# Kernel tuning notes

Hardware: AMD Instinct MI355X
Metric: run time of the kernel (lower is better)

## Reference

```python
import jax, jax.numpy as jnp
import numpy as np

STEPS = 250
BETA = 0.02


def setup_inputs() -> dict:
    key = jax.random.key(0)
    k1, k2 = jax.random.split(key)
    reflectance_normal = jax.random.normal(k1, (8, 1024, 1024), dtype=jnp.float32)
    distribution = jax.random.normal(k2, (8, 65536), dtype=jnp.float32)
    return {"reflectance_normal": reflectance_normal, "distribution": distribution}


def reference(reflectance_normal, distribution):
    # Faithful vectorized version of ForwardDiffusionModel.forward:
    # per batch element, 250 steps of xt = sqrt(1-b)*xt + sqrt(b)*sample,
    # where sample is drawn i.i.d. uniformly (with replacement) from the
    # flattened empirical distribution values of that batch element.
    B = reflectance_normal.shape[0]
    flat = distribution.reshape(B, -1)          # [B, N]
    N = flat.shape[1]
    a = np.sqrt(1.0 - BETA).astype(np.float32)
    b = np.sqrt(BETA).astype(np.float32)
    sample_shape = reflectance_normal.shape     # [B, H, W]

    keys = jax.random.split(jax.random.key(42), STEPS)

    def step(xt, k):
        idx = jax.random.randint(k, sample_shape, 0, N)                 # [B,H,W]
        sample = jnp.take_along_axis(flat, idx.reshape(B, -1), axis=1)  # [B,H*W]
        sample = sample.reshape(sample_shape)
        return a * xt + b * sample, None

    xt, _ = jax.lax.scan(step, reflectance_normal, keys)
    return xt
```

## Files before the change

kernel.cpp:

```cpp
#include <hip/hip_runtime.h>
#include <hip/hip_fp16.h>
#include <stdint.h>

#define NDIST 65536
#define NSTEPS 250

#define TF_ROUND(r) { x0 += x1; x1 = (x1 << (r)) | (x1 >> (32 - (r))); x1 ^= x0; }

__device__ __forceinline__ uint2 threefry2x32(uint32_t ks0, uint32_t ks1, uint32_t ks2,
                                              uint32_t x0, uint32_t x1) {
  x0 += ks0; x1 += ks1;
  TF_ROUND(13) TF_ROUND(15) TF_ROUND(26) TF_ROUND(6)
  x0 += ks1; x1 += ks2 + 1u;
  TF_ROUND(17) TF_ROUND(29) TF_ROUND(16) TF_ROUND(24)
  x0 += ks2; x1 += ks0 + 2u;
  TF_ROUND(13) TF_ROUND(15) TF_ROUND(26) TF_ROUND(6)
  x0 += ks0; x1 += ks1 + 3u;
  TF_ROUND(17) TF_ROUND(29) TF_ROUND(16) TF_ROUND(24)
  x0 += ks1; x1 += ks2 + 4u;
  TF_ROUND(13) TF_ROUND(15) TF_ROUND(26) TF_ROUND(6)
  x0 += ks2; x1 += ks0 + 5u;
  return make_uint2(x0, x1);
}

__device__ __forceinline__ void init_keys(uint32_t* keys, int tid) {
  if (tid < NSTEPS) {
    uint2 ks = threefry2x32(0u, 42u, 0x1BD11BDAu ^ 42u, 0u, (uint32_t)tid);
    uint2 k2 = threefry2x32(ks.x, ks.y, ks.x ^ ks.y ^ 0x1BD11BDAu, 0u, 1u);
    keys[2 * tid]     = k2.x;
    keys[2 * tid + 1] = k2.y;
  }
}

#define WGL 1024
#define GL  8

__global__ __launch_bounds__(WGL, 1) void fwd_diff_full(
    const float* __restrict__ x_init,
    const float* __restrict__ dist,
    float* __restrict__ out) {
  extern __shared__ char smem[];
  __half*   tab  = reinterpret_cast<__half*>(smem);
  uint32_t* keys = reinterpret_cast<uint32_t*>(smem + 131072);

  const int tid   = threadIdx.x;
  const int batch = blockIdx.x >> 7;
  const int chunk = blockIdx.x & 127;
  const uint32_t base = ((uint32_t)batch << 20) + ((uint32_t)chunk << 13);

  const float Ac = 0.9899494936611665f;
  const float Bc = 0.1414213562373095f;

  const float4* src = reinterpret_cast<const float4*>(dist + (size_t)batch * NDIST);
  for (int i = tid; i < NDIST / 4; i += WGL) {
    float4 v = src[i];
    ushort4 h;
    h.x = __half_as_ushort(__float2half(Bc * v.x));
    h.y = __half_as_ushort(__float2half(Bc * v.y));
    h.z = __half_as_ushort(__float2half(Bc * v.z));
    h.w = __half_as_ushort(__float2half(Bc * v.w));
    reinterpret_cast<ushort4*>(tab)[i] = h;
  }
  init_keys(keys, tid);
  __syncthreads();

  uint32_t p[GL];
  float acc[GL];
#pragma unroll
  for (int j = 0; j < GL; ++j) {
    p[j]   = base + (uint32_t)(j * WGL) + (uint32_t)tid;
    acc[j] = x_init[p[j]];
  }

  for (int s = 0; s < NSTEPS; ++s) {
    uint32_t kx = keys[2 * s];
    uint32_t ky = keys[2 * s + 1];
    kx = (uint32_t)__builtin_amdgcn_readfirstlane((int)kx);
    ky = (uint32_t)__builtin_amdgcn_readfirstlane((int)ky);
    const uint32_t kz = kx ^ ky ^ 0x1BD11BDAu;
#pragma unroll
    for (int j = 0; j < GL; ++j) {
      uint2 r = threefry2x32(kx, ky, kz, 0u, p[j]);
      uint32_t idx = r.y & 0xFFFFu;
      acc[j] = fmaf(Ac, acc[j], __half2float(tab[idx]));
    }
  }

#pragma unroll
  for (int j = 0; j < GL; ++j) out[p[j]] = acc[j];
}

#define WGH 512
#define GH  8
#define NLDS 31744

__global__ __launch_bounds__(WGH, 1) void fwd_diff_hyb(
    const float* __restrict__ x_init,
    const float* __restrict__ dist,
    float* __restrict__ out) {
  __shared__ __half   tab[NLDS];
  __shared__ uint32_t keys[2 * NSTEPS];

  const int tid   = threadIdx.x;
  const int batch = blockIdx.x >> 8;
  const int chunk = blockIdx.x & 255;
  const uint32_t base = ((uint32_t)batch << 20) + ((uint32_t)chunk << 12);

  const float Ac = 0.9899494936611665f;
  const float Bc = 0.1414213562373095f;

  const float* __restrict__ row = dist + (size_t)batch * NDIST;

  const float4* src4 = reinterpret_cast<const float4*>(row);
  for (int i = tid; i < NLDS / 4; i += WGH) {
    float4 v = src4[i];
    ushort4 h;
    h.x = __half_as_ushort(__float2half(Bc * v.x));
    h.y = __half_as_ushort(__float2half(Bc * v.y));
    h.z = __half_as_ushort(__float2half(Bc * v.z));
    h.w = __half_as_ushort(__float2half(Bc * v.w));
    *reinterpret_cast<ushort4*>(&tab[i * 4]) = h;
  }
  init_keys(keys, tid);
  __syncthreads();

  uint32_t p[GH];
  float acc[GH];
#pragma unroll
  for (int j = 0; j < GH; ++j) {
    p[j]   = base + (uint32_t)(j * WGH) + (uint32_t)tid;
    acc[j] = x_init[p[j]];
  }

  for (int s = 0; s < NSTEPS; ++s) {
    uint32_t kx = keys[2 * s];
    uint32_t ky = keys[2 * s + 1];
    kx = (uint32_t)__builtin_amdgcn_readfirstlane((int)kx);
    ky = (uint32_t)__builtin_amdgcn_readfirstlane((int)ky);
    const uint32_t kz = kx ^ ky ^ 0x1BD11BDAu;
#pragma unroll
    for (int j = 0; j < GH; ++j) {
      uint2 r = threefry2x32(kx, ky, kz, 0u, p[j]);
      uint32_t idx = r.y & 0xFFFFu;
      float sv;
      if (idx < NLDS) sv = __half2float(tab[idx]);
      else            sv = Bc * row[idx];
      acc[j] = fmaf(Ac, acc[j], sv);
    }
  }

#pragma unroll
  for (int j = 0; j < GH; ++j) out[p[j]] = acc[j];
}

extern "C" void kernel_launch(void* const* d_in, const int* in_sizes, int n_in,
                              void* d_out, int out_size, void* d_ws, size_t ws_size,
                              hipStream_t stream) {
  const float* x_init = (const float*)d_in[0];
  const float* dist   = (const float*)d_in[1];
  if (n_in >= 2 && in_sizes[0] == 8 * NDIST) {
    x_init = (const float*)d_in[1];
    dist   = (const float*)d_in[0];
  }
  float* out = (float*)d_out;

  const int smem_bytes = 131072 + 2048;

  hipError_t st = hipFuncSetAttribute(
      reinterpret_cast<const void*>(fwd_diff_full),
      hipFuncAttributeMaxDynamicSharedMemorySize, smem_bytes);
  int max_blocks = 0;
  if (st == hipSuccess) {
    st = hipOccupancyMaxActiveBlocksPerMultiprocessor(
        &max_blocks, reinterpret_cast<const void*>(fwd_diff_full), WGL, smem_bytes);
  }

  if (st == hipSuccess && max_blocks >= 1) {
    fwd_diff_full<<<dim3(1024), dim3(WGL), smem_bytes, stream>>>(x_init, dist, out);
  } else {
    fwd_diff_hyb<<<dim3(2048), dim3(WGH), 0, stream>>>(x_init, dist, out);
  }
}
```

Before: 3.556 ms.

## Precompute step keys in separate kernel and double per-thread work per block

Adds a small kernel that computes the 250 per-step Threefry keys once into workspace, so the main kernel reads them from global memory (uniform scalar loads) instead of building them per block in LDS. The main kernel now processes 16 elements per thread with 512 blocks, which halves how often each batch's 128KB half-precision table is reloaded. Hash computation is split from the table gathers so the loads can be batched, and rotations use a rotate builtin. The risk is higher register pressure with 16 live states and fewer blocks than CUs, which could leave some CUs idle.

```diff
diff --git a/kernel.cpp b/kernel.cpp
--- a/kernel.cpp
+++ b/kernel.cpp
@@ -5,7 +5,13 @@
 #define NDIST 65536
 #define NSTEPS 250
 
-#define TF_ROUND(r) { x0 += x1; x1 = (x1 << (r)) | (x1 >> (32 - (r))); x1 ^= x0; }
+#if __has_builtin(__builtin_rotateleft32)
+#define ROTL(x, r) __builtin_rotateleft32((x), (r))
+#else
+#define ROTL(x, r) (((x) << (r)) | ((x) >> (32 - (r))))
+#endif
+
+#define TF_ROUND(r) { x0 += x1; x1 = ROTL(x1, r); x1 ^= x0; }
 
 __device__ __forceinline__ uint2 threefry2x32(uint32_t ks0, uint32_t ks1, uint32_t ks2,
                                               uint32_t x0, uint32_t x1) {
@@ -23,24 +29,84 @@
   return make_uint2(x0, x1);
 }
 
-__device__ __forceinline__ void init_keys(uint32_t* keys, int tid) {
+
+__global__ void keys_kernel(uint32_t* __restrict__ ks_out) {
+  const int tid = threadIdx.x;
   if (tid < NSTEPS) {
     uint2 ks = threefry2x32(0u, 42u, 0x1BD11BDAu ^ 42u, 0u, (uint32_t)tid);
     uint2 k2 = threefry2x32(ks.x, ks.y, ks.x ^ ks.y ^ 0x1BD11BDAu, 0u, 1u);
-    keys[2 * tid]     = k2.x;
-    keys[2 * tid + 1] = k2.y;
+    ks_out[2 * tid]     = k2.x;
+    ks_out[2 * tid + 1] = k2.y;
   }
 }
 
 #define WGL 1024
-#define GL  8
+#define GL  16
+
+__global__ __launch_bounds__(WGL, 1) void fwd_diff_v2(
+    const float* __restrict__ x_init,
+    const float* __restrict__ dist,
+    const uint32_t* __restrict__ keysg,
+    float* __restrict__ out) {
+  extern __shared__ __half tab[];
+
+  const int tid   = threadIdx.x;
+  const int batch = blockIdx.x >> 6;
+  const int chunk = blockIdx.x & 63;
+  const uint32_t base = ((uint32_t)batch << 20) + ((uint32_t)chunk << 14);
+
+  const float Ac = 0.9899494936611665f;
+  const float Bc = 0.1414213562373095f;
+
+  const float4* src = reinterpret_cast<const float4*>(dist + (size_t)batch * NDIST);
+  for (int i = tid; i < NDIST / 4; i += WGL) {
+    float4 v = src[i];
+    ushort4 h;
+    h.x = __half_as_ushort(__float2half(Bc * v.x));
+    h.y = __half_as_ushort(__float2half(Bc * v.y));
+    h.z = __half_as_ushort(__float2half(Bc * v.z));
+    h.w = __half_as_ushort(__float2half(Bc * v.w));
+    reinterpret_cast<ushort4*>(tab)[i] = h;
+  }
+  __syncthreads();
+
+  uint32_t p[GL];
+  float acc[GL];
+#pragma unroll
+  for (int j = 0; j < GL; ++j) {
+    p[j]   = base + (uint32_t)(j * WGL) + (uint32_t)tid;
+    acc[j] = x_init[p[j]];
+  }
+
+  for (int s = 0; s < NSTEPS; ++s) {
+    const uint32_t kx = keysg[2 * s];
+    const uint32_t ky = keysg[2 * s + 1];
+    const uint32_t kz = kx ^ ky ^ 0x1BD11BDAu;
+
+    uint32_t idx[GL];
+#pragma unroll
+    for (int j = 0; j < GL; ++j) {
+      uint2 r = threefry2x32(kx, ky, kz, 0u, p[j]);
+      idx[j] = r.y & 0xFFFFu;
+    }
+#pragma unroll
+    for (int j = 0; j < GL; ++j) {
+      acc[j] = fmaf(Ac, acc[j], __half2float(tab[idx[j]]));
+    }
+  }
+
+#pragma unroll
+  for (int j = 0; j < GL; ++j) out[p[j]] = acc[j];
+}
+
+#define GF9 8
 
 __global__ __launch_bounds__(WGL, 1) void fwd_diff_full(
     const float* __restrict__ x_init,
     const float* __restrict__ dist,
     float* __restrict__ out) {
   extern __shared__ char smem[];
-  __half*   tab  = reinterpret_cast<__half*>(smem);
+  __half*   tab9 = reinterpret_cast<__half*>(smem);
   uint32_t* keys = reinterpret_cast<uint32_t*>(smem + 131072);
 
   const int tid   = threadIdx.x;
@@ -59,15 +125,20 @@
     h.y = __half_as_ushort(__float2half(Bc * v.y));
     h.z = __half_as_ushort(__float2half(Bc * v.z));
     h.w = __half_as_ushort(__float2half(Bc * v.w));
-    reinterpret_cast<ushort4*>(tab)[i] = h;
+    reinterpret_cast<ushort4*>(tab9)[i] = h;
   }
-  init_keys(keys, tid);
+  if (tid < NSTEPS) {
+    uint2 ks = threefry2x32(0u, 42u, 0x1BD11BDAu ^ 42u, 0u, (uint32_t)tid);
+    uint2 k2 = threefry2x32(ks.x, ks.y, ks.x ^ ks.y ^ 0x1BD11BDAu, 0u, 1u);
+    keys[2 * tid]     = k2.x;
+    keys[2 * tid + 1] = k2.y;
+  }
   __syncthreads();
 
-  uint32_t p[GL];
-  float acc[GL];
+  uint32_t p[GF9];
+  float acc[GF9];
 #pragma unroll
-  for (int j = 0; j < GL; ++j) {
+  for (int j = 0; j < GF9; ++j) {
     p[j]   = base + (uint32_t)(j * WGL) + (uint32_t)tid;
     acc[j] = x_init[p[j]];
   }
@@ -79,78 +150,15 @@
     ky = (uint32_t)__builtin_amdgcn_readfirstlane((int)ky);
     const uint32_t kz = kx ^ ky ^ 0x1BD11BDAu;
 #pragma unroll
-    for (int j = 0; j < GL; ++j) {
+    for (int j = 0; j < GF9; ++j) {
       uint2 r = threefry2x32(kx, ky, kz, 0u, p[j]);
       uint32_t idx = r.y & 0xFFFFu;
-      acc[j] = fmaf(Ac, acc[j], __half2float(tab[idx]));
+      acc[j] = fmaf(Ac, acc[j], __half2float(tab9[idx]));
     }
   }
 
 #pragma unroll
-  for (int j = 0; j < GL; ++j) out[p[j]] = acc[j];
-}
-
-#define WGH 512
-#define GH  8
-#define NLDS 31744
-
-__global__ __launch_bounds__(WGH, 1) void fwd_diff_hyb(
-    const float* __restrict__ x_init,
-    const float* __restrict__ dist,
-    float* __restrict__ out) {
-  __shared__ __half   tab[NLDS];
-  __shared__ uint32_t keys[2 * NSTEPS];
-
-  const int tid   = threadIdx.x;
-  const int batch = blockIdx.x >> 8;
-  const int chunk = blockIdx.x & 255;
-  const uint32_t base = ((uint32_t)batch << 20) + ((uint32_t)chunk << 12);
-
-  const float Ac = 0.9899494936611665f;
-  const float Bc = 0.1414213562373095f;
-
-  const float* __restrict__ row = dist + (size_t)batch * NDIST;
-
-  const float4* src4 = reinterpret_cast<const float4*>(row);
-  for (int i = tid; i < NLDS / 4; i += WGH) {
-    float4 v = src4[i];
-    ushort4 h;
-    h.x = __half_as_ushort(__float2half(Bc * v.x));
-    h.y = __half_as_ushort(__float2half(Bc * v.y));
-    h.z = __half_as_ushort(__float2half(Bc * v.z));
-    h.w = __half_as_ushort(__float2half(Bc * v.w));
-    *reinterpret_cast<ushort4*>(&tab[i * 4]) = h;
-  }
-  init_keys(keys, tid);
-  __syncthreads();
-
-  uint32_t p[GH];
-  float acc[GH];
-#pragma unroll
-  for (int j = 0; j < GH; ++j) {
-    p[j]   = base + (uint32_t)(j * WGH) + (uint32_t)tid;
-    acc[j] = x_init[p[j]];
-  }
-
-  for (int s = 0; s < NSTEPS; ++s) {
-    uint32_t kx = keys[2 * s];
-    uint32_t ky = keys[2 * s + 1];
-    kx = (uint32_t)__builtin_amdgcn_readfirstlane((int)kx);
-    ky = (uint32_t)__builtin_amdgcn_readfirstlane((int)ky);
-    const uint32_t kz = kx ^ ky ^ 0x1BD11BDAu;
-#pragma unroll
-    for (int j = 0; j < GH; ++j) {
-      uint2 r = threefry2x32(kx, ky, kz, 0u, p[j]);
-      uint32_t idx = r.y & 0xFFFFu;
-      float sv;
-      if (idx < NLDS) sv = __half2float(tab[idx]);
-      else            sv = Bc * row[idx];
-      acc[j] = fmaf(Ac, acc[j], sv);
-    }
-  }
-
-#pragma unroll
-  for (int j = 0; j < GH; ++j) out[p[j]] = acc[j];
+  for (int j = 0; j < GF9; ++j) out[p[j]] = acc[j];
 }
 
 extern "C" void kernel_launch(void* const* d_in, const int* in_sizes, int n_in,
@@ -163,21 +171,26 @@
     dist   = (const float*)d_in[0];
   }
   float* out = (float*)d_out;
+  uint32_t* keysg = (uint32_t*)d_ws;
 
-  const int smem_bytes = 131072 + 2048;
+  const int smem_v2 = 131072;
 
   hipError_t st = hipFuncSetAttribute(
-      reinterpret_cast<const void*>(fwd_diff_full),
-      hipFuncAttributeMaxDynamicSharedMemorySize, smem_bytes);
+      reinterpret_cast<const void*>(fwd_diff_v2),
+      hipFuncAttributeMaxDynamicSharedMemorySize, smem_v2);
   int max_blocks = 0;
   if (st == hipSuccess) {
     st = hipOccupancyMaxActiveBlocksPerMultiprocessor(
-        &max_blocks, reinterpret_cast<const void*>(fwd_diff_full), WGL, smem_bytes);
+        &max_blocks, reinterpret_cast<const void*>(fwd_diff_v2), WGL, smem_v2);
   }
 
-  if (st == hipSuccess && max_blocks >= 1) {
-    fwd_diff_full<<<dim3(1024), dim3(WGL), smem_bytes, stream>>>(x_init, dist, out);
+  if (st == hipSuccess && max_blocks >= 1 && ws_size >= 2 * NSTEPS * sizeof(uint32_t)) {
+    keys_kernel<<<dim3(1), dim3(256), 0, stream>>>(keysg);
+    fwd_diff_v2<<<dim3(512), dim3(WGL), smem_v2, stream>>>(x_init, dist, keysg, out);
   } else {
-    fwd_diff_hyb<<<dim3(2048), dim3(WGH), 0, stream>>>(x_init, dist, out);
+    const int smem_v1 = 131072 + 2048;
+    (void)hipFuncSetAttribute(reinterpret_cast<const void*>(fwd_diff_full),
+                              hipFuncAttributeMaxDynamicSharedMemorySize, smem_v1);
+    fwd_diff_full<<<dim3(1024), dim3(WGL), smem_v1, stream>>>(x_init, dist, out);
   }
 }
```

Measured after the change: 3.543 ms. Within noise of the previous version (-0.4%).
